# Performance work log

Hardware: AMD Instinct MI355X
Metric: run time of the kernel (lower is better)

The kernel has to match this reference:

```python
import jax, jax.numpy as jnp
import numpy as np

B, T, C = 1, 2048, 2048
H, G, HS = 32, 8, 64          # heads, query groups, head size
FF = 5632                     # LLaMAMLP intermediate size
EPS = 1e-5
LEVELS = 63.0                 # 2**6 - 1 (bit=6)


@jax.custom_vjp
def _uq(x, alpha):
    xd = x / alpha
    xq = jnp.round(jnp.clip(xd, 0.0, 1.0) * LEVELS) / LEVELS
    return xq * alpha


def _uq_fwd(x, alpha):
    xd = x / alpha
    xq = jnp.round(jnp.clip(xd, 0.0, 1.0) * LEVELS) / LEVELS
    return xq * alpha, (xd, xq)


def _uq_bwd(res, g):
    xd, xq = res
    i = (xd > 1.0).astype(g.dtype)
    grad_x = g * (1.0 - i)
    grad_alpha = jnp.sum(g * (i + (xq - xd) * (1.0 - i)))
    return grad_x, grad_alpha


_uq.defvjp(_uq_fwd, _uq_bwd)


def quant_relu(x, alpha):
    return _uq(jax.nn.relu(x), alpha)


def rmsnorm(x, w):
    return w * x * jax.lax.rsqrt(jnp.mean(x * x, axis=-1, keepdims=True) + EPS)


def setup_inputs() -> dict:
    key = jax.random.key(0)
    ks = jax.random.split(key, 8)
    s = 0.02
    shape_qkv = (H + 2 * G) * HS  # 3072
    return {
        "x": jax.random.normal(ks[0], (B, T, C), jnp.float32),
        "w_rms1": jnp.ones((C,), jnp.float32),
        "w_rms2": jnp.ones((C,), jnp.float32),
        "alpha1": jnp.asarray(8.0, jnp.float32),
        "alpha2": jnp.asarray(8.0, jnp.float32),
        "alpha_q": jnp.asarray(8.0, jnp.float32),
        "alpha_sm": jnp.asarray(8.0, jnp.float32),
        "attn_w": jax.random.normal(ks[1], (shape_qkv, C), jnp.float32) * s,
        "proj_w": jax.random.normal(ks[2], (C, C), jnp.float32) * s,
        "fc1_w": jax.random.normal(ks[3], (FF, C), jnp.float32) * s,
        "fc2_w": jax.random.normal(ks[4], (FF, C), jnp.float32) * s,
        "mlp_proj_w": jax.random.normal(ks[5], (C, FF), jnp.float32) * s,
        "max_seq_length": 2048,
    }


def _attention(n1, attn_w, proj_w, alpha_q, alpha_sm):
    q_per_kv = H // G
    qkv = quant_relu(jnp.einsum('btc,oc->bto', n1, attn_w), alpha_q)
    qkv = qkv.reshape(B, T, G, q_per_kv + 2, HS)
    q = qkv[..., :q_per_kv, :].reshape(B, T, H, HS)
    k = qkv[..., q_per_kv, :]      # [B,T,G,HS]
    v = qkv[..., q_per_kv + 1, :]  # [B,T,G,HS]
    k = jnp.repeat(k, q_per_kv, axis=2)  # [B,T,H,HS]
    v = jnp.repeat(v, q_per_kv, axis=2)
    scale = 1.0 / np.sqrt(HS).astype(np.float32)
    scores = jnp.einsum('bqhd,bkhd->bhqk', q, k) * scale
    causal = jnp.tril(jnp.ones((T, T), bool))
    scores = jnp.where(causal, scores, jnp.float32(-jnp.inf))
    w = jax.nn.softmax(scores, axis=-1)
    w = quant_relu(w, alpha_sm)  # quantized softmax weights (QuantReLU on probs)
    y = jnp.einsum('bhqk,bkhd->bqhd', w, v).reshape(B, T, C)
    return jnp.einsum('btc,oc->bto', y, proj_w)


def reference(x, w_rms1, w_rms2, alpha1, alpha2, attn_w, proj_w, alpha_q,
              alpha_sm, fc1_w, fc2_w, mlp_proj_w, max_seq_length):
    n1 = quant_relu(rmsnorm(x, w_rms1), alpha1)
    h = _attention(n1, attn_w, proj_w, alpha_q, alpha_sm)
    x = x + h
    n2 = quant_relu(rmsnorm(x, w_rms2), alpha2)
    gate = jax.nn.silu(jnp.einsum('btc,fc->btf', n2, fc1_w))
    up = jnp.einsum('btc,fc->btf', n2, fc2_w)
    mlp = jnp.einsum('btf,cf->btc', gate * up, mlp_proj_w)
    return x + mlp
```

## Files before the change

kernel.cpp:

```cpp
#include <hip/hip_runtime.h>
#include <hip/hip_bf16.h>
#include <math.h>


#define T_SEQ 2048
#define C_DIM 2048
#define QKV_DIM 3072
#define FF_DIM 5632
#define FF_HALF 2816

typedef short bf16x8 __attribute__((ext_vector_type(8)));
typedef float f32x4 __attribute__((ext_vector_type(4)));
typedef unsigned short u16;
typedef unsigned int u32;

__device__ __forceinline__ u16 f2bf(float f) {
  __hip_bfloat16 h = __float2bfloat16(f);
  return *reinterpret_cast<u16*>(&h);
}
__device__ __forceinline__ float bf2f(u16 u) {
  __hip_bfloat16 h;
  *reinterpret_cast<u16*>(&h) = u;
  return __bfloat162float(h);
}

__device__ __forceinline__ float qint(float v, float alpha) {
  float xd = fmaxf(v, 0.0f) / alpha;
  xd = fminf(xd, 1.0f);
  return rintf(xd * 63.0f);
}

__device__ __forceinline__ void llds16(const void* g, void* l) {
  __builtin_amdgcn_global_load_lds(
      (const __attribute__((address_space(1))) unsigned int*)g,
      (__attribute__((address_space(3))) unsigned int*)l, 16, 0, 0);
}

__global__ __launch_bounds__(256) void rmsnorm_quant_int(const float* __restrict__ x,
                                                         const float* __restrict__ w,
                                                         const float* __restrict__ alpha_p,
                                                         u16* __restrict__ out) {
  const int row = blockIdx.x;
  const float* xr = x + (size_t)row * C_DIM;
  const int base = threadIdx.x * 8;
  float4 v0 = *reinterpret_cast<const float4*>(xr + base);
  float4 v1 = *reinterpret_cast<const float4*>(xr + base + 4);
  float xv[8] = {v0.x, v0.y, v0.z, v0.w, v1.x, v1.y, v1.z, v1.w};
  float ss = 0.0f;
#pragma unroll
  for (int k = 0; k < 8; ++k) ss = fmaf(xv[k], xv[k], ss);
#pragma unroll
  for (int m = 1; m < 64; m <<= 1) ss += __shfl_xor(ss, m);
  __shared__ float wsum[4];
  const int lane = threadIdx.x & 63, wv = threadIdx.x >> 6;
  if (lane == 0) wsum[wv] = ss;
  __syncthreads();
  const float tot = wsum[0] + wsum[1] + wsum[2] + wsum[3];
  const float rs = 1.0f / sqrtf(tot * (1.0f / 2048.0f) + 1e-5f);
  const float alpha = *alpha_p;
  u16 ov[8];
#pragma unroll
  for (int k = 0; k < 8; ++k) ov[k] = f2bf(qint((w[base + k] * xv[k]) * rs, alpha));
  u16* orow = out + (size_t)row * C_DIM + base;
#pragma unroll
  for (int k = 0; k < 2; ++k) {
    ushort4 u;
    u.x = ov[k * 4]; u.y = ov[k * 4 + 1]; u.z = ov[k * 4 + 2]; u.w = ov[k * 4 + 3];
    *reinterpret_cast<ushort4*>(orow + k * 4) = u;
  }
}

__global__ __launch_bounds__(256) void conv_split(const float* __restrict__ src, int ld,
                                                  int cols,
                                                  u16* __restrict__ hi, u16* __restrict__ lo) {
  const int r = blockIdx.x;
  const int c4 = (blockIdx.y * 256 + threadIdx.x) * 4;
  if (c4 >= cols) return;
  float4 v = *reinterpret_cast<const float4*>(&src[(size_t)r * ld + c4]);
  float f[4] = {v.x, v.y, v.z, v.w};
  ushort4 h, l;
  u16 hh[4], ll[4];
#pragma unroll
  for (int j = 0; j < 4; ++j) {
    hh[j] = f2bf(f[j]);
    ll[j] = f2bf(f[j] - bf2f(hh[j]));
  }
  h.x = hh[0]; h.y = hh[1]; h.z = hh[2]; h.w = hh[3];
  l.x = ll[0]; l.y = ll[1]; l.z = ll[2]; l.w = ll[3];
  const size_t o = (size_t)r * cols + c4;
  *reinterpret_cast<ushort4*>(&hi[o]) = h;
  *reinterpret_cast<ushort4*>(&lo[o]) = l;
}

template <int MODE, int EPI>
__global__ __launch_bounds__(256) void gemm_mfma(
    const u16* __restrict__ A0, const u16* __restrict__ A1,
    const u16* __restrict__ B0, const u16* __restrict__ B1,
    float* __restrict__ Cf, u16* __restrict__ Cq, const float* __restrict__ auxf,
    u16* __restrict__ p_hi, u16* __restrict__ p_lo,
    const float* __restrict__ sA_p, const float* __restrict__ aQ_p,
    int M, int N, int K) {
  constexpr int NT = (MODE == 2) ? 3 : 4;
  __shared__ __align__(16) u16 lds[NT * 4096];

  const int tid = threadIdx.x;
  const int nwg = gridDim.x * gridDim.y;
  const int wg = blockIdx.y * gridDim.x + blockIdx.x;
  const int swz = (wg & 7) * (nwg >> 3) + (wg >> 3);
  const int bx = swz % gridDim.x, by = swz / gridDim.x;
  const int row0 = by * 128, col0 = bx * 128;

  const int w = tid >> 6, lane = tid & 63;
  const int wr = w >> 1, wc = w & 1;
  const int fr = lane & 15, ko = (lane >> 4) * 8;

  const int c0 = w * 128 + lane;
  const int r_a = c0 >> 2;
  const int s_a = (c0 & 3) * 8;

  u16* tA0 = lds;
  u16* tX1 = lds + 4096;
  u16* tX2 = lds + 8192;
  u16* tX3 = (MODE == 3) ? lds + 12288 : lds;

  f32x4 acc[4][4];
  const f32x4 zero = {0.f, 0.f, 0.f, 0.f};
#pragma unroll
  for (int m = 0; m < 4; ++m)
#pragma unroll
    for (int n = 0; n < 4; ++n) acc[m][n] = zero;

  for (int kt = 0; kt < K; kt += 32) {
    __syncthreads();
    {
      const u16* g0 = A0 + (size_t)(row0 + r_a) * K + kt + s_a;
      const u16* g1 = A0 + (size_t)(row0 + r_a + 16) * K + kt + s_a;
      llds16(g0, tA0 + (w * 128) * 8);
      llds16(g1, tA0 + (w * 128 + 64) * 8);
    }
    if constexpr (MODE == 3) {
      const u16* g0 = A1 + (size_t)(row0 + r_a) * K + kt + s_a;
      const u16* g1 = A1 + (size_t)(row0 + r_a + 16) * K + kt + s_a;
      llds16(g0, tX1 + (w * 128) * 8);
      llds16(g1, tX1 + (w * 128 + 64) * 8);
    }
    {
      u16* dst = (MODE == 2) ? tX1 : tX2;
      const u16* g0 = B0 + (size_t)(col0 + r_a) * K + kt + s_a;
      const u16* g1 = B0 + (size_t)(col0 + r_a + 16) * K + kt + s_a;
      llds16(g0, dst + (w * 128) * 8);
      llds16(g1, dst + (w * 128 + 64) * 8);
    }
    {
      u16* dst = (MODE == 2) ? tX2 : tX3;
      const u16* g0 = B1 + (size_t)(col0 + r_a) * K + kt + s_a;
      const u16* g1 = B1 + (size_t)(col0 + r_a + 16) * K + kt + s_a;
      llds16(g0, dst + (w * 128) * 8);
      llds16(g1, dst + (w * 128 + 64) * 8);
    }
    __syncthreads();

    bf16x8 a0f[4], bhf[4], blf[4];
    const u16* Bhi = (MODE == 2) ? tX1 : tX2;
    const u16* Blo = (MODE == 2) ? tX2 : tX3;
#pragma unroll
    for (int m = 0; m < 4; ++m)
      a0f[m] = *reinterpret_cast<const bf16x8*>(&tA0[(wr * 64 + m * 16 + fr) * 32 + ko]);
#pragma unroll
    for (int n = 0; n < 4; ++n) {
      bhf[n] = *reinterpret_cast<const bf16x8*>(&Bhi[(wc * 64 + n * 16 + fr) * 32 + ko]);
      blf[n] = *reinterpret_cast<const bf16x8*>(&Blo[(wc * 64 + n * 16 + fr) * 32 + ko]);
    }
    if constexpr (MODE == 2) {
#pragma unroll
      for (int m = 0; m < 4; ++m)
#pragma unroll
        for (int n = 0; n < 4; ++n) {
          acc[m][n] = __builtin_amdgcn_mfma_f32_16x16x32_bf16(a0f[m], bhf[n], acc[m][n], 0, 0, 0);
          acc[m][n] = __builtin_amdgcn_mfma_f32_16x16x32_bf16(a0f[m], blf[n], acc[m][n], 0, 0, 0);
        }
    } else {
      bf16x8 a1f[4];
#pragma unroll
      for (int m = 0; m < 4; ++m)
        a1f[m] = *reinterpret_cast<const bf16x8*>(&tX1[(wr * 64 + m * 16 + fr) * 32 + ko]);
#pragma unroll
      for (int m = 0; m < 4; ++m)
#pragma unroll
        for (int n = 0; n < 4; ++n) {
          acc[m][n] = __builtin_amdgcn_mfma_f32_16x16x32_bf16(a0f[m], bhf[n], acc[m][n], 0, 0, 0);
          acc[m][n] = __builtin_amdgcn_mfma_f32_16x16x32_bf16(a1f[m], bhf[n], acc[m][n], 0, 0, 0);
          acc[m][n] = __builtin_amdgcn_mfma_f32_16x16x32_bf16(a0f[m], blf[n], acc[m][n], 0, 0, 0);
        }
    }
  }

  float sA = 1.0f, aQ = 1.0f;
  if constexpr (EPI == 1) { sA = (*sA_p) * (1.0f / 63.0f); aQ = *aQ_p; }
  if constexpr (EPI == 2 || EPI == 3) { sA = (*sA_p) * (1.0f / 63.0f); }
#pragma unroll
  for (int m = 0; m < 4; ++m)
#pragma unroll
    for (int n = 0; n < 4; ++n) {
      const int gcol = col0 + wc * 64 + n * 16 + fr;
#pragma unroll
      for (int j = 0; j < 4; ++j) {
        const int grow = row0 + wr * 64 + m * 16 + (lane >> 4) * 4 + j;
        const size_t idx = (size_t)grow * N + gcol;
        const float v = acc[m][n][j];
        if constexpr (EPI == 0) {
          Cf[idx] = auxf[idx] + v;
        } else if constexpr (EPI == 1) {
          float t = v * sA;
          float xd = fminf(fmaxf(t, 0.0f) / aQ, 1.0f);
          Cq[idx] = f2bf(rintf(xd * 63.0f));
        } else if constexpr (EPI == 2) {
          float t = v * sA;
          u16 h = f2bf(t);
          p_hi[idx] = h;
          p_lo[idx] = f2bf(t - bf2f(h));
        } else if constexpr (EPI == 3) {
          float gg = bf2f(p_hi[idx]) + bf2f(p_lo[idx]);
          float u = v * sA;
          float gu = (gg / (1.0f + expf(-gg))) * u;
          u16 h = f2bf(gu);
          p_hi[idx] = h;
          p_lo[idx] = f2bf(gu - bf2f(h));
        }
      }
    }
}

__global__ __launch_bounds__(256) void v_transpose(const u16* __restrict__ qkv,
                                                   u16* __restrict__ vt) {
  const int tb = blockIdx.x, g = blockIdx.y;
  const int vcol = (g * 6 + 5) * 64;
  __shared__ u16 t[64][72];
  const int tid = threadIdx.x;
#pragma unroll
  for (int i = 0; i < 2; ++i) {
    const int ch = i * 256 + tid;
    const int row = ch >> 3, c8 = (ch & 7) * 8;
    bf16x8 v = *reinterpret_cast<const bf16x8*>(
        qkv + (size_t)(tb * 64 + row) * QKV_DIM + vcol + c8);
#pragma unroll
    for (int j = 0; j < 8; ++j) t[c8 + j][row] = (u16)v[j];
  }
  __syncthreads();
#pragma unroll
  for (int i = 0; i < 2; ++i) {
    const int ch = i * 256 + tid;
    const int hs = ch >> 3, t8 = (ch & 7) * 8;
    ushort4 a, b;
    a.x = t[hs][t8];     a.y = t[hs][t8 + 1]; a.z = t[hs][t8 + 2]; a.w = t[hs][t8 + 3];
    b.x = t[hs][t8 + 4]; b.y = t[hs][t8 + 5]; b.z = t[hs][t8 + 6]; b.w = t[hs][t8 + 7];
    u16* dst = vt + (size_t)(g * 64 + hs) * T_SEQ + tb * 64 + t8;
    *reinterpret_cast<ushort4*>(dst) = a;
    *reinterpret_cast<ushort4*>(dst + 4) = b;
  }
}

__global__ __launch_bounds__(256) void attn_fused(const u16* __restrict__ qkv,
                                                  const u16* __restrict__ vt,
                                                  u16* __restrict__ y_hi,
                                                  u16* __restrict__ y_lo,
                                                  const float* __restrict__ aq_p,
                                                  const float* __restrict__ asm_p) {
  const int c = blockIdx.x;
  const int chi = c >> 8, mid = (c >> 4) & 15, clo = c & 15;
  const int h = mid + (chi << 4);
  const int qb = chi ? (15 - clo) : clo;
  const int g = h >> 2, s = h & 3;
  const int q_col = (g * 6 + s) * 64;
  const int k_col = (g * 6 + 4) * 64;

  __shared__ __align__(16) char lds_raw[49152];
  u16* Ks  = (u16*)(lds_raw + 16384);
  u16* Vts = (u16*)(lds_raw + 24576);

  const int tid = threadIdx.x;
  const int w = tid >> 6, lane = tid & 63;
  const int fr = lane & 15, gg = lane >> 4;
  char* myW = lds_raw + 32768 + w * 4096;

  const float sq = (*aq_p) * (1.0f / 63.0f);
  const float scale = sq * sq * 0.125f;
  const float alpha_sm = *asm_p;
  const float scale_y = (alpha_sm * (1.0f / 63.0f)) * sq;
  const int nkt = 2 * qb + 2;

#pragma unroll
  for (int i = 0; i < 4; ++i) {
    const int cb = (w * 4 + i) * 64;
    const int ch = cb + lane;
    const int row = ch >> 3;
    const int sb = ((ch & 7) * 16) ^ ((row & 7) << 4);
    llds16(qkv + (size_t)(qb * 128 + row) * QKV_DIM + q_col + (sb >> 1),
           lds_raw + cb * 16);
  }
  __syncthreads();
  bf16x8 qf[2][2];
#pragma unroll
  for (int nq = 0; nq < 2; ++nq)
#pragma unroll
    for (int ks = 0; ks < 2; ++ks) {
      const int qr = w * 32 + nq * 16 + fr;
      qf[nq][ks] = *reinterpret_cast<const bf16x8*>(
          lds_raw + ((qr * 128 + ks * 64 + gg * 16) ^ ((qr & 7) << 4)));
    }

  float m_run[2] = {-INFINITY, -INFINITY};
  float l_run[2] = {0.0f, 0.0f};

  for (int kt = 0; kt < nkt; ++kt) {
    __syncthreads();
#pragma unroll
    for (int i = 0; i < 2; ++i) {
      const int cb = (w * 2 + i) * 64;
      const int ch = cb + lane;
      const int row = ch >> 3;
      const int sb = ((ch & 7) * 16) ^ ((row & 7) << 4);
      llds16(qkv + (size_t)(kt * 64 + row) * QKV_DIM + k_col + (sb >> 1),
             (char*)Ks + cb * 16);
    }
    __syncthreads();
    f32x4 sac[4][2];
    const f32x4 zero = {0.f, 0.f, 0.f, 0.f};
#pragma unroll
    for (int mk = 0; mk < 4; ++mk)
#pragma unroll
      for (int nq = 0; nq < 2; ++nq) sac[mk][nq] = zero;
#pragma unroll
    for (int ks = 0; ks < 2; ++ks)
#pragma unroll
      for (int mk = 0; mk < 4; ++mk) {
        const int kr = mk * 16 + fr;
        bf16x8 kf = *reinterpret_cast<const bf16x8*>(
            (char*)Ks + ((kr * 128 + ks * 64 + gg * 16) ^ ((kr & 7) << 4)));
#pragma unroll
        for (int nq = 0; nq < 2; ++nq)
          sac[mk][nq] = __builtin_amdgcn_mfma_f32_16x16x32_bf16(kf, qf[nq][ks], sac[mk][nq], 0, 0, 0);
      }
    const bool edge = (kt >= 2 * qb);
#pragma unroll
    for (int nq = 0; nq < 2; ++nq) {
      const int qglob = qb * 128 + w * 32 + nq * 16 + fr;
      float vm = -INFINITY;
#pragma unroll
      for (int mk = 0; mk < 4; ++mk)
#pragma unroll
        for (int jj = 0; jj < 4; ++jj) {
          float sv = sac[mk][nq][jj] * scale;
          if (edge && (kt * 64 + mk * 16 + gg * 4 + jj > qglob)) sv = -INFINITY;
          vm = fmaxf(vm, sv);
        }
      vm = fmaxf(vm, __shfl_xor(vm, 16));
      vm = fmaxf(vm, __shfl_xor(vm, 32));
      const float mn = fmaxf(m_run[nq], vm);
      float p = 0.0f;
#pragma unroll
      for (int mk = 0; mk < 4; ++mk)
#pragma unroll
        for (int jj = 0; jj < 4; ++jj) {
          float sv = sac[mk][nq][jj] * scale;
          if (edge && (kt * 64 + mk * 16 + gg * 4 + jj > qglob)) sv = -INFINITY;
          p += expf(sv - mn);
        }
      p += __shfl_xor(p, 16);
      p += __shfl_xor(p, 32);
      l_run[nq] = l_run[nq] * expf(m_run[nq] - mn) + p;
      m_run[nq] = mn;
    }
  }

  const float linv[2] = {1.0f / l_run[0], 1.0f / l_run[1]};
  f32x4 oac[4][2];
  {
    const f32x4 zero = {0.f, 0.f, 0.f, 0.f};
#pragma unroll
    for (int mh = 0; mh < 4; ++mh)
#pragma unroll
      for (int nq = 0; nq < 2; ++nq) oac[mh][nq] = zero;
  }

  for (int kt = 0; kt < nkt; ++kt) {
    __syncthreads();
#pragma unroll
    for (int i = 0; i < 2; ++i) {
      const int cb = (w * 2 + i) * 64;
      const int ch = cb + lane;
      const int row = ch >> 3;
      const int sb = ((ch & 7) * 16) ^ ((row & 7) << 4);
      llds16(qkv + (size_t)(kt * 64 + row) * QKV_DIM + k_col + (sb >> 1),
             (char*)Ks + cb * 16);
      llds16(vt + (size_t)(g * 64 + row) * T_SEQ + kt * 64 + (sb >> 1),
             (char*)Vts + cb * 16);
    }
    __syncthreads();
    f32x4 sac[4][2];
    const f32x4 zero = {0.f, 0.f, 0.f, 0.f};
#pragma unroll
    for (int mk = 0; mk < 4; ++mk)
#pragma unroll
      for (int nq = 0; nq < 2; ++nq) sac[mk][nq] = zero;
#pragma unroll
    for (int ks = 0; ks < 2; ++ks)
#pragma unroll
      for (int mk = 0; mk < 4; ++mk) {
        const int kr = mk * 16 + fr;
        bf16x8 kf = *reinterpret_cast<const bf16x8*>(
            (char*)Ks + ((kr * 128 + ks * 64 + gg * 16) ^ ((kr & 7) << 4)));
#pragma unroll
        for (int nq = 0; nq < 2; ++nq)
          sac[mk][nq] = __builtin_amdgcn_mfma_f32_16x16x32_bf16(kf, qf[nq][ks], sac[mk][nq], 0, 0, 0);
      }
    const bool edge = (kt >= 2 * qb);
#pragma unroll
    for (int nq = 0; nq < 2; ++nq) {
      const int qglob = qb * 128 + w * 32 + nq * 16 + fr;
      const int qloc = nq * 16 + fr;
      const float mr = m_run[nq], li = linv[nq];
#pragma unroll
      for (int mk = 0; mk < 4; ++mk) {
        u32 pk[2];
#pragma unroll
        for (int dd = 0; dd < 2; ++dd) {
          u32 lo16, hi16;
          {
            float sv = sac[mk][nq][dd * 2] * scale;
            if (edge && (kt * 64 + mk * 16 + gg * 4 + dd * 2 > qglob)) sv = -INFINITY;
            float wv = expf(sv - mr) * li;
            lo16 = f2bf(rintf(fminf(wv / alpha_sm, 1.0f) * 63.0f));
          }
          {
            float sv = sac[mk][nq][dd * 2 + 1] * scale;
            if (edge && (kt * 64 + mk * 16 + gg * 4 + dd * 2 + 1 > qglob)) sv = -INFINITY;
            float wv = expf(sv - mr) * li;
            hi16 = f2bf(rintf(fminf(wv / alpha_sm, 1.0f) * 63.0f));
          }
          pk[dd] = (hi16 << 16) | lo16;
        }
        const int b0 = (qloc * 128 + (mk * 16 + gg * 4) * 2) ^ ((qloc & 7) << 4);
        *reinterpret_cast<u32*>(myW + b0) = pk[0];
        *reinterpret_cast<u32*>(myW + b0 + 4) = pk[1];
      }
    }
#pragma unroll
    for (int ks = 0; ks < 2; ++ks) {
      bf16x8 wf[2];
#pragma unroll
      for (int nq = 0; nq < 2; ++nq) {
        const int qloc = nq * 16 + fr;
        wf[nq] = *reinterpret_cast<const bf16x8*>(
            myW + ((qloc * 128 + ks * 64 + gg * 16) ^ ((qloc & 7) << 4)));
      }
#pragma unroll
      for (int mh = 0; mh < 4; ++mh) {
        const int hr = mh * 16 + fr;
        bf16x8 vf = *reinterpret_cast<const bf16x8*>(
            (char*)Vts + ((hr * 128 + ks * 64 + gg * 16) ^ ((hr & 7) << 4)));
#pragma unroll
        for (int nq = 0; nq < 2; ++nq)
          oac[mh][nq] = __builtin_amdgcn_mfma_f32_16x16x32_bf16(vf, wf[nq], oac[mh][nq], 0, 0, 0);
      }
    }
  }

  __syncthreads();
  float* osc = (float*)(lds_raw + w * 8192);
#pragma unroll
  for (int mh = 0; mh < 4; ++mh)
#pragma unroll
    for (int nq = 0; nq < 2; ++nq) {
      const int qloc = nq * 16 + fr;
#pragma unroll
      for (int jj = 0; jj < 4; ++jj) {
        const int hs = mh * 16 + gg * 4 + jj;
        *reinterpret_cast<float*>(
            (char*)osc + ((qloc * 256 + hs * 4) ^ ((qloc & 7) << 4))) =
            oac[mh][nq][jj] * scale_y;
      }
    }
  __syncthreads();
  const int qp = lane >> 1, hf = lane & 1;
  const int qrow = qb * 128 + w * 32 + qp;
  u16* dh = y_hi + (size_t)qrow * C_DIM + h * 64 + hf * 32;
  u16* dl = y_lo + (size_t)qrow * C_DIM + h * 64 + hf * 32;
#pragma unroll
  for (int u = 0; u < 8; ++u) {
    f32x4 v = *reinterpret_cast<const f32x4*>(
        (char*)osc + ((qp * 256 + hf * 128 + u * 16) ^ ((qp & 7) << 4)));
    ushort4 hh, ll;
    u16 t0 = f2bf(v[0]); hh.x = t0; ll.x = f2bf(v[0] - bf2f(t0));
    u16 t1 = f2bf(v[1]); hh.y = t1; ll.y = f2bf(v[1] - bf2f(t1));
    u16 t2 = f2bf(v[2]); hh.z = t2; ll.z = f2bf(v[2] - bf2f(t2));
    u16 t3 = f2bf(v[3]); hh.w = t3; ll.w = f2bf(v[3] - bf2f(t3));
    *reinterpret_cast<ushort4*>(dh + u * 4) = hh;
    *reinterpret_cast<ushort4*>(dl + u * 4) = ll;
  }
}

extern "C" void kernel_launch(void* const* d_in, const int* in_sizes, int n_in,
                              void* d_out, int out_size, void* d_ws, size_t ws_size,
                              hipStream_t stream) {
  (void)in_sizes; (void)n_in; (void)out_size; (void)ws_size;
  const float* x      = (const float*)d_in[0];
  const float* w1     = (const float*)d_in[1];
  const float* w2     = (const float*)d_in[2];
  const float* a1     = (const float*)d_in[3];
  const float* a2     = (const float*)d_in[4];
  const float* aq     = (const float*)d_in[5];
  const float* a_sm   = (const float*)d_in[6];
  const float* attn_w = (const float*)d_in[7];
  const float* proj_w = (const float*)d_in[8];
  const float* fc1_w  = (const float*)d_in[9];
  const float* fc2_w  = (const float*)d_in[10];
  const float* mlp_w  = (const float*)d_in[11];
  float* out = (float*)d_out;

  char* ws = (char*)d_ws;
  u16* Whi   = (u16*)ws;
  u16* nb    = (u16*)(ws + 25165824);
  char* A    = ws + 33554432;
  u16* qkv_i = (u16*)A;
  u16* y_hi  = (u16*)(A + 12582912);
  u16* y_lo  = (u16*)(A + 20971520);
  u16* vt    = (u16*)(A + 29360128);
  u16* ghi   = (u16*)A;
  u16* glo   = (u16*)(A + 11534336);

  rmsnorm_quant_int<<<T_SEQ, 256, 0, stream>>>(x, w1, a1, nb);
  conv_split<<<dim3(QKV_DIM, 2), 256, 0, stream>>>(attn_w, C_DIM, C_DIM,
                                                   Whi, Whi + (size_t)QKV_DIM * C_DIM);
  gemm_mfma<2, 1><<<dim3(QKV_DIM / 128, T_SEQ / 128), 256, 0, stream>>>(
      nb, nullptr, Whi, Whi + (size_t)QKV_DIM * C_DIM, nullptr, qkv_i, nullptr,
      nullptr, nullptr, a1, aq, T_SEQ, QKV_DIM, C_DIM);
  v_transpose<<<dim3(32, 8), 256, 0, stream>>>(qkv_i, vt);
  attn_fused<<<512, 256, 0, stream>>>(qkv_i, vt, y_hi, y_lo, aq, a_sm);
  conv_split<<<dim3(C_DIM, 2), 256, 0, stream>>>(proj_w, C_DIM, C_DIM,
                                                 Whi, Whi + (size_t)C_DIM * C_DIM);
  gemm_mfma<3, 0><<<dim3(C_DIM / 128, T_SEQ / 128), 256, 0, stream>>>(
      y_hi, y_lo, Whi, Whi + (size_t)C_DIM * C_DIM, out, nullptr, x,
      nullptr, nullptr, nullptr, nullptr, T_SEQ, C_DIM, C_DIM);
  rmsnorm_quant_int<<<T_SEQ, 256, 0, stream>>>(out, w2, a2, nb);
  for (int h = 0; h < 2; ++h) {
    const float* fc1h = fc1_w + (size_t)h * FF_HALF * C_DIM;
    const float* fc2h = fc2_w + (size_t)h * FF_HALF * C_DIM;
    const float* mlph = mlp_w + (size_t)h * FF_HALF;
    conv_split<<<dim3(FF_HALF, 2), 256, 0, stream>>>(fc1h, C_DIM, C_DIM,
                                                     Whi, Whi + (size_t)FF_HALF * C_DIM);
    gemm_mfma<2, 2><<<dim3(FF_HALF / 128, T_SEQ / 128), 256, 0, stream>>>(
        nb, nullptr, Whi, Whi + (size_t)FF_HALF * C_DIM, nullptr, nullptr, nullptr,
        ghi, glo, a2, nullptr, T_SEQ, FF_HALF, C_DIM);
    conv_split<<<dim3(FF_HALF, 2), 256, 0, stream>>>(fc2h, C_DIM, C_DIM,
                                                     Whi, Whi + (size_t)FF_HALF * C_DIM);
    gemm_mfma<2, 3><<<dim3(FF_HALF / 128, T_SEQ / 128), 256, 0, stream>>>(
        nb, nullptr, Whi, Whi + (size_t)FF_HALF * C_DIM, nullptr, nullptr, nullptr,
        ghi, glo, a2, nullptr, T_SEQ, FF_HALF, C_DIM);
    conv_split<<<dim3(C_DIM, 3), 256, 0, stream>>>(mlph, FF_DIM, FF_HALF,
                                                   Whi, Whi + (size_t)C_DIM * FF_HALF);
    gemm_mfma<3, 0><<<dim3(C_DIM / 128, T_SEQ / 128), 256, 0, stream>>>(
        ghi, glo, Whi, Whi + (size_t)C_DIM * FF_HALF, out, nullptr, out,
        nullptr, nullptr, nullptr, nullptr, T_SEQ, C_DIM, FF_HALF);
  }
}
```

Measured before the change: 1.184 ms.

## Double-buffer GEMM LDS tiles and use hardware exp2 with packed bf16 conversion in attention

```diff
diff --git a/kernel.cpp b/kernel.cpp
--- a/kernel.cpp
+++ b/kernel.cpp
@@ -8,6 +8,7 @@
 #define QKV_DIM 3072
 #define FF_DIM 5632
 #define FF_HALF 2816
+#define LOG2E 1.44269504088896340736f
 
 typedef short bf16x8 __attribute__((ext_vector_type(8)));
 typedef float f32x4 __attribute__((ext_vector_type(4)));
@@ -28,6 +29,17 @@
   float xd = fmaxf(v, 0.0f) / alpha;
   xd = fminf(xd, 1.0f);
   return rintf(xd * 63.0f);
+}
+
+__device__ __forceinline__ float exp2_hw(float x) {
+  float r;
+  asm("v_exp_f32 %0, %1" : "=v"(r) : "v"(x));
+  return r;
+}
+__device__ __forceinline__ u32 cvtpk_bf16(float lo, float hi) {
+  u32 r;
+  asm("v_cvt_pk_bf16_f32 %0, %1, %2" : "=v"(r) : "v"(lo), "v"(hi));
+  return r;
 }
 
 __device__ __forceinline__ void llds16(const void* g, void* l) {
@@ -101,7 +113,7 @@
     const float* __restrict__ sA_p, const float* __restrict__ aQ_p,
     int M, int N, int K) {
   constexpr int NT = (MODE == 2) ? 3 : 4;
-  __shared__ __align__(16) u16 lds[NT * 4096];
+  __shared__ __align__(16) u16 lds[2 * NT * 4096];
 
   const int tid = threadIdx.x;
   const int nwg = gridDim.x * gridDim.y;
@@ -118,51 +130,56 @@
   const int r_a = c0 >> 2;
   const int s_a = (c0 & 3) * 8;
 
-  u16* tA0 = lds;
-  u16* tX1 = lds + 4096;
-  u16* tX2 = lds + 8192;
-  u16* tX3 = (MODE == 3) ? lds + 12288 : lds;
-
-  f32x4 acc[4][4];
-  const f32x4 zero = {0.f, 0.f, 0.f, 0.f};
-#pragma unroll
-  for (int m = 0; m < 4; ++m)
-#pragma unroll
-    for (int n = 0; n < 4; ++n) acc[m][n] = zero;
-
-  for (int kt = 0; kt < K; kt += 32) {
-    __syncthreads();
+  u16* cu = lds;
+  u16* nx = lds + NT * 4096;
+
+  auto stage = [&](u16* base, int kt) {
     {
       const u16* g0 = A0 + (size_t)(row0 + r_a) * K + kt + s_a;
       const u16* g1 = A0 + (size_t)(row0 + r_a + 16) * K + kt + s_a;
-      llds16(g0, tA0 + (w * 128) * 8);
-      llds16(g1, tA0 + (w * 128 + 64) * 8);
+      llds16(g0, base + (w * 128) * 8);
+      llds16(g1, base + (w * 128 + 64) * 8);
     }
     if constexpr (MODE == 3) {
       const u16* g0 = A1 + (size_t)(row0 + r_a) * K + kt + s_a;
       const u16* g1 = A1 + (size_t)(row0 + r_a + 16) * K + kt + s_a;
-      llds16(g0, tX1 + (w * 128) * 8);
-      llds16(g1, tX1 + (w * 128 + 64) * 8);
+      llds16(g0, base + 4096 + (w * 128) * 8);
+      llds16(g1, base + 4096 + (w * 128 + 64) * 8);
     }
     {
-      u16* dst = (MODE == 2) ? tX1 : tX2;
+      u16* dst = base + ((MODE == 2) ? 4096 : 8192);
       const u16* g0 = B0 + (size_t)(col0 + r_a) * K + kt + s_a;
       const u16* g1 = B0 + (size_t)(col0 + r_a + 16) * K + kt + s_a;
       llds16(g0, dst + (w * 128) * 8);
       llds16(g1, dst + (w * 128 + 64) * 8);
     }
     {
-      u16* dst = (MODE == 2) ? tX2 : tX3;
+      u16* dst = base + ((MODE == 2) ? 8192 : 12288);
       const u16* g0 = B1 + (size_t)(col0 + r_a) * K + kt + s_a;
       const u16* g1 = B1 + (size_t)(col0 + r_a + 16) * K + kt + s_a;
       llds16(g0, dst + (w * 128) * 8);
       llds16(g1, dst + (w * 128 + 64) * 8);
     }
-    __syncthreads();
-
+  };
+
+  f32x4 acc[4][4];
+  const f32x4 zero = {0.f, 0.f, 0.f, 0.f};
+#pragma unroll
+  for (int m = 0; m < 4; ++m)
+#pragma unroll
+    for (int n = 0; n < 4; ++n) acc[m][n] = zero;
+
+  stage(cu, 0);
+  __syncthreads();
+
+  for (int kt = 0;; kt += 32) {
+    const bool more = (kt + 32 < K);
+    if (more) stage(nx, kt + 32);
+
+    const u16* tA0 = cu;
+    const u16* Bhi = cu + ((MODE == 2) ? 4096 : 8192);
+    const u16* Blo = cu + ((MODE == 2) ? 8192 : 12288);
     bf16x8 a0f[4], bhf[4], blf[4];
-    const u16* Bhi = (MODE == 2) ? tX1 : tX2;
-    const u16* Blo = (MODE == 2) ? tX2 : tX3;
 #pragma unroll
     for (int m = 0; m < 4; ++m)
       a0f[m] = *reinterpret_cast<const bf16x8*>(&tA0[(wr * 64 + m * 16 + fr) * 32 + ko]);
@@ -183,7 +200,7 @@
       bf16x8 a1f[4];
 #pragma unroll
       for (int m = 0; m < 4; ++m)
-        a1f[m] = *reinterpret_cast<const bf16x8*>(&tX1[(wr * 64 + m * 16 + fr) * 32 + ko]);
+        a1f[m] = *reinterpret_cast<const bf16x8*>(&cu[4096 + (wr * 64 + m * 16 + fr) * 32 + ko]);
 #pragma unroll
       for (int m = 0; m < 4; ++m)
 #pragma unroll
@@ -193,6 +210,9 @@
           acc[m][n] = __builtin_amdgcn_mfma_f32_16x16x32_bf16(a0f[m], blf[n], acc[m][n], 0, 0, 0);
         }
     }
+    if (!more) break;
+    __syncthreads();
+    u16* t = cu; cu = nx; nx = t;
   }
 
   float sA = 1.0f, aQ = 1.0f;
@@ -284,8 +304,9 @@
   char* myW = lds_raw + 32768 + w * 4096;
 
   const float sq = (*aq_p) * (1.0f / 63.0f);
-  const float scale = sq * sq * 0.125f;
+  const float scale2 = sq * sq * 0.125f * LOG2E;
   const float alpha_sm = *asm_p;
+  const float inv_a63 = 63.0f / alpha_sm;
   const float scale_y = (alpha_sm * (1.0f / 63.0f)) * sq;
   const int nkt = 2 * qb + 2;
 
@@ -345,30 +366,27 @@
 #pragma unroll
     for (int nq = 0; nq < 2; ++nq) {
       const int qglob = qb * 128 + w * 32 + nq * 16 + fr;
-      float vm = -INFINITY;
+      float tv[16];
 #pragma unroll
       for (int mk = 0; mk < 4; ++mk)
 #pragma unroll
         for (int jj = 0; jj < 4; ++jj) {
-          float sv = sac[mk][nq][jj] * scale;
-          if (edge && (kt * 64 + mk * 16 + gg * 4 + jj > qglob)) sv = -INFINITY;
-          vm = fmaxf(vm, sv);
+          float t = sac[mk][nq][jj] * scale2;
+          if (edge && (kt * 64 + mk * 16 + gg * 4 + jj > qglob)) t = -INFINITY;
+          tv[mk * 4 + jj] = t;
         }
+      float vm = tv[0];
+#pragma unroll
+      for (int i = 1; i < 16; ++i) vm = fmaxf(vm, tv[i]);
       vm = fmaxf(vm, __shfl_xor(vm, 16));
       vm = fmaxf(vm, __shfl_xor(vm, 32));
       const float mn = fmaxf(m_run[nq], vm);
       float p = 0.0f;
 #pragma unroll
-      for (int mk = 0; mk < 4; ++mk)
-#pragma unroll
-        for (int jj = 0; jj < 4; ++jj) {
-          float sv = sac[mk][nq][jj] * scale;
-          if (edge && (kt * 64 + mk * 16 + gg * 4 + jj > qglob)) sv = -INFINITY;
-          p += expf(sv - mn);
-        }
+      for (int i = 0; i < 16; ++i) p += exp2_hw(tv[i] - mn);
       p += __shfl_xor(p, 16);
       p += __shfl_xor(p, 32);
-      l_run[nq] = l_run[nq] * expf(m_run[nq] - mn) + p;
+      l_run[nq] = l_run[nq] * exp2_hw(m_run[nq] - mn) + p;
       m_run[nq] = mn;
     }
   }
@@ -419,30 +437,22 @@
     for (int nq = 0; nq < 2; ++nq) {
       const int qglob = qb * 128 + w * 32 + nq * 16 + fr;
       const int qloc = nq * 16 + fr;
-      const float mr = m_run[nq], li = linv[nq];
+      const float mr = m_run[nq];
+      const float cw = linv[nq] * inv_a63;
 #pragma unroll
       for (int mk = 0; mk < 4; ++mk) {
-        u32 pk[2];
-#pragma unroll
-        for (int dd = 0; dd < 2; ++dd) {
-          u32 lo16, hi16;
-          {
-            float sv = sac[mk][nq][dd * 2] * scale;
-            if (edge && (kt * 64 + mk * 16 + gg * 4 + dd * 2 > qglob)) sv = -INFINITY;
-            float wv = expf(sv - mr) * li;
-            lo16 = f2bf(rintf(fminf(wv / alpha_sm, 1.0f) * 63.0f));
-          }
-          {
-            float sv = sac[mk][nq][dd * 2 + 1] * scale;
-            if (edge && (kt * 64 + mk * 16 + gg * 4 + dd * 2 + 1 > qglob)) sv = -INFINITY;
-            float wv = expf(sv - mr) * li;
-            hi16 = f2bf(rintf(fminf(wv / alpha_sm, 1.0f) * 63.0f));
-          }
-          pk[dd] = (hi16 << 16) | lo16;
+        float lv[4];
+#pragma unroll
+        for (int jj = 0; jj < 4; ++jj) {
+          float t = sac[mk][nq][jj] * scale2;
+          if (edge && (kt * 64 + mk * 16 + gg * 4 + jj > qglob)) t = -INFINITY;
+          lv[jj] = rintf(fminf(exp2_hw(t - mr) * cw, 63.0f));
         }
+        const u32 pk0 = cvtpk_bf16(lv[0], lv[1]);
+        const u32 pk1 = cvtpk_bf16(lv[2], lv[3]);
         const int b0 = (qloc * 128 + (mk * 16 + gg * 4) * 2) ^ ((qloc & 7) << 4);
-        *reinterpret_cast<u32*>(myW + b0) = pk[0];
-        *reinterpret_cast<u32*>(myW + b0 + 4) = pk[1];
+        *reinterpret_cast<u32*>(myW + b0) = pk0;
+        *reinterpret_cast<u32*>(myW + b0 + 4) = pk1;
       }
     }
 #pragma unroll
```

New measurement: 1.008 ms. 1.17x faster.
